# Optimization experiments

Measured on AMD Instinct MI355X. Metric: run time of the kernel, lower is better.

Reference implementation:

```python
import jax, jax.numpy as jnp
import numpy as np

N = 8192
D_IN = 128
D_OUT = 128


def setup_inputs() -> dict:
    key = jax.random.key(0)
    k1, k2, k3 = jax.random.split(key, 3)
    x = jax.random.normal(k1, (N, D_IN), dtype=jnp.float32)
    adj = jax.random.uniform(k2, (N, N), dtype=jnp.float32)  # dense adjacency / edge weights
    weight = jax.random.normal(k3, (D_IN, D_OUT), dtype=jnp.float32) * (1.0 / np.sqrt(D_IN))
    bias = jnp.zeros((D_OUT,), dtype=jnp.float32)
    return {"x": x, "adj": adj, "weight": weight, "bias": bias}


def gcn_norm(adj, add_self_loops=False):
    # symmetric normalization: D^{-1/2} A D^{-1/2}
    if add_self_loops:
        adj = adj + jnp.eye(adj.shape[0], dtype=adj.dtype)
    deg = adj.sum(axis=1)
    dinv = jnp.where(deg > 0, jax.lax.rsqrt(deg), 0.0)  # masked_fill(isinf, 0)
    return adj * dinv[:, None] * dinv[None, :]


def reference(x, adj, weight, bias):
    adj_n = gcn_norm(adj, add_self_loops=False)  # cached normalized adjacency
    h = x @ weight                               # [N, D_out] dense projection
    out = adj_n @ h + bias                       # neighborhood aggregation + bias
    return out
```

## Files before the change

### kernel.cpp

```cpp
#include <hip/hip_runtime.h>
#include <hip/hip_bf16.h>

#define NN 8192
#define DD 128

typedef __attribute__((ext_vector_type(4))) float f32x4;
typedef __attribute__((ext_vector_type(8))) short s16x8;
typedef __attribute__((ext_vector_type(4))) short s16x4;

__device__ inline short bfbits(float f) {
    unsigned u = __builtin_bit_cast(unsigned, f);
    u += 0x7fffu + ((u >> 16) & 1u);
    return (short)(u >> 16);
}

__device__ inline s16x4 cvt4(f32x4 a) {
    s16x4 r;
    r[0] = bfbits(a[0]); r[1] = bfbits(a[1]); r[2] = bfbits(a[2]); r[3] = bfbits(a[3]);
    return r;
}

__device__ inline s16x8 cvt8(f32x4 a, f32x4 b) {
    s16x8 r;
    r[0] = bfbits(a[0]); r[1] = bfbits(a[1]); r[2] = bfbits(a[2]); r[3] = bfbits(a[3]);
    r[4] = bfbits(b[0]); r[5] = bfbits(b[1]); r[6] = bfbits(b[2]); r[7] = bfbits(b[3]);
    return r;
}

__global__ __launch_bounds__(256) void deg_kernel(const float* __restrict__ adj,
                                                  float* __restrict__ dinv) {
    const int lane = threadIdx.x & 63;
    const int row  = (blockIdx.x << 2) + (threadIdx.x >> 6);
    const float* r = adj + (size_t)row * NN;

    f32x4 s = {0.f, 0.f, 0.f, 0.f};
    #pragma unroll 4
    for (int it = 0; it < 32; ++it) {
        f32x4 v = *(const f32x4*)(r + it * 256 + (lane << 2));
        s += v;
    }
    float sum = s[0] + s[1] + s[2] + s[3];
    #pragma unroll
    for (int off = 32; off; off >>= 1) sum += __shfl_xor(sum, off, 64);
    if (lane == 0) dinv[row] = (sum > 0.f) ? rsqrtf(sum) : 0.f;
}

#define WST 132
__global__ __launch_bounds__(256) void proj_kernel(const float* __restrict__ x,
                                                   const float* __restrict__ w,
                                                   const float* __restrict__ dinv,
                                                   unsigned short* __restrict__ h2f) {
    __shared__ short lds_w[128 * WST];
    const int tid  = threadIdx.x;
    const int lane = tid & 63;
    const int wave = tid >> 6;
    const int j0   = blockIdx.x << 4;
    const int n0   = wave << 5;
    const int r    = lane & 15;
    const int q    = lane >> 4;

    #pragma unroll
    for (int i = 0; i < 16; ++i) {
        int gi = i * 256 + tid;
        int k  = gi >> 5;
        int n4 = (gi & 31) << 2;
        f32x4 v = *(const f32x4*)(w + (size_t)k * DD + n4);
        *(s16x4*)&lds_w[k * WST + n4] = cvt4(v);
    }
    __syncthreads();

    const float* xp = x + (size_t)(j0 + r) * DD + (q << 3);

    f32x4 acc0 = {0.f, 0.f, 0.f, 0.f};
    f32x4 acc1 = {0.f, 0.f, 0.f, 0.f};

    #pragma unroll
    for (int k = 0; k < DD; k += 32) {
        f32x4 a0 = *(const f32x4*)(xp + k);
        f32x4 a1 = *(const f32x4*)(xp + k + 4);
        s16x8 af = cvt8(a0, a1);

        const int kb = k + (q << 3);
        s16x8 b0, b1;
        #pragma unroll
        for (int jj = 0; jj < 8; ++jj) {
            b0[jj] = lds_w[(kb + jj) * WST + n0 + r];
            b1[jj] = lds_w[(kb + jj) * WST + n0 + 16 + r];
        }
        acc0 = __builtin_amdgcn_mfma_f32_16x16x32_bf16(af, b0, acc0, 0, 0, 0);
        acc1 = __builtin_amdgcn_mfma_f32_16x16x32_bf16(af, b1, acc1, 0, 0, 0);
    }

    #pragma unroll
    for (int rr = 0; rr < 4; ++rr) {
        const int j = j0 + (q << 2) + rr;
        const float dv = dinv[j];
        const int kg = j >> 5, qp = (j >> 3) & 3, jj = j & 7;
        #pragma unroll
        for (int half = 0; half < 2; ++half) {
            const int n = n0 + half * 16 + r;
            const int f = n >> 4;
            const int lanep = qp * 16 + (n & 15);
            const float v = (half ? acc1[rr] : acc0[rr]) * dv;
            h2f[((((size_t)f << 8) + kg) << 6 | lanep) * 8 + jj] = (unsigned short)bfbits(v);
        }
    }
}

template <int KSPLIT>
__global__ __launch_bounds__(256, 4) void agg32_kernel(const float* __restrict__ adj,
                                                       const unsigned short* __restrict__ h2f,
                                                       float* __restrict__ dst) {
    constexpr int KS    = NN / KSPLIT;
    constexpr int TILES = KS / 128;
    __shared__ short lds_a[2][2][16 * 16 * 8];

    const int tid  = threadIdx.x;
    const int lane = tid & 63;
    const int wave = tid >> 6;
    const int r    = lane & 15;
    const int q    = lane >> 4;
    const int m0   = blockIdx.x << 5;
    const int k0   = blockIdx.y * KS;

    const int row0 = tid >> 5;
    const int off0 = (tid & 31) << 2;
    const int cd   = (tid & 31) >> 1;
    const int hh   = tid & 1;
    const int so0  = ((row0 << 4) + (cd ^ row0)) * 8 + hh * 4;
    const int so1  = (((8 + row0) << 4) + (cd ^ (8 + row0))) * 8 + hh * 4;

    const float* ap0 = adj + (size_t)(m0 + row0)      * NN + k0 + off0;
    const float* ap1 = adj + (size_t)(m0 + 8 + row0)  * NN + k0 + off0;
    const float* ap2 = adj + (size_t)(m0 + 16 + row0) * NN + k0 + off0;
    const float* ap3 = adj + (size_t)(m0 + 24 + row0) * NN + k0 + off0;

    const unsigned short* bb0 = h2f + (((size_t)(wave * 2)     * 256 + (k0 >> 5)) * 64 + lane) * 8;
    const unsigned short* bb1 = h2f + (((size_t)(wave * 2 + 1) * 256 + (k0 >> 5)) * 64 + lane) * 8;

    f32x4 acc00 = {0.f, 0.f, 0.f, 0.f};
    f32x4 acc01 = {0.f, 0.f, 0.f, 0.f};
    f32x4 acc10 = {0.f, 0.f, 0.f, 0.f};
    f32x4 acc11 = {0.f, 0.f, 0.f, 0.f};

    {
        f32x4 v0 = *(const f32x4*)(ap0);
        f32x4 v1 = *(const f32x4*)(ap1);
        f32x4 v2 = *(const f32x4*)(ap2);
        f32x4 v3 = *(const f32x4*)(ap3);
        *(s16x4*)&lds_a[0][0][so0] = cvt4(v0);
        *(s16x4*)&lds_a[0][0][so1] = cvt4(v1);
        *(s16x4*)&lds_a[0][1][so0] = cvt4(v2);
        *(s16x4*)&lds_a[0][1][so1] = cvt4(v3);
    }
    __syncthreads();

    for (int t = 0; t < TILES; ++t) {
        const short* lc0 = lds_a[t & 1][0];
        const short* lc1 = lds_a[t & 1][1];

        s16x8 br0[4], br1[4];
        #pragma unroll
        for (int s = 0; s < 4; ++s) {
            br0[s] = *(const s16x8*)(bb0 + (size_t)(t * 4 + s) * 512);
            br1[s] = *(const s16x8*)(bb1 + (size_t)(t * 4 + s) * 512);
        }
        f32x4 v0, v1, v2, v3;
        if (t + 1 < TILES) {
            v0 = *(const f32x4*)(ap0 + (t + 1) * 128);
            v1 = *(const f32x4*)(ap1 + (t + 1) * 128);
            v2 = *(const f32x4*)(ap2 + (t + 1) * 128);
            v3 = *(const f32x4*)(ap3 + (t + 1) * 128);
        }
        #pragma unroll
        for (int s = 0; s < 4; ++s) {
            const int slot = (r << 4) + (((s << 2) + q) ^ r);
            s16x8 afA = *(const s16x8*)(lc0 + slot * 8);
            s16x8 afB = *(const s16x8*)(lc1 + slot * 8);
            acc00 = __builtin_amdgcn_mfma_f32_16x16x32_bf16(afA, br0[s], acc00, 0, 0, 0);
            acc01 = __builtin_amdgcn_mfma_f32_16x16x32_bf16(afA, br1[s], acc01, 0, 0, 0);
            acc10 = __builtin_amdgcn_mfma_f32_16x16x32_bf16(afB, br0[s], acc10, 0, 0, 0);
            acc11 = __builtin_amdgcn_mfma_f32_16x16x32_bf16(afB, br1[s], acc11, 0, 0, 0);
        }
        if (t + 1 < TILES) {
            short* ln0 = (short*)lds_a[(t + 1) & 1][0];
            short* ln1 = (short*)lds_a[(t + 1) & 1][1];
            *(s16x4*)(ln0 + so0) = cvt4(v0);
            *(s16x4*)(ln0 + so1) = cvt4(v1);
            *(s16x4*)(ln1 + so0) = cvt4(v2);
            *(s16x4*)(ln1 + so1) = cvt4(v3);
        }
        __syncthreads();
    }

    float* p = dst + (size_t)blockIdx.y * NN * DD;
    #pragma unroll
    for (int rr = 0; rr < 4; ++rr) {
        const int mA = m0 + (q << 2) + rr;
        const int mB = mA + 16;
        const int n  = (wave << 5) + r;
        p[(size_t)mA * DD + n]      = acc00[rr];
        p[(size_t)mA * DD + n + 16] = acc01[rr];
        p[(size_t)mB * DD + n]      = acc10[rr];
        p[(size_t)mB * DD + n + 16] = acc11[rr];
    }
}

template <int KSPLIT>
__global__ __launch_bounds__(256, 4) void agg_kernel(const float* __restrict__ adj,
                                                     const unsigned short* __restrict__ h2f,
                                                     const float* __restrict__ dinv,
                                                     const float* __restrict__ bias,
                                                     float* __restrict__ dst) {
    constexpr int KS    = NN / KSPLIT;
    constexpr int TILES = KS / 128;
    __shared__ short lds_a[2][16 * 16 * 8];

    const int tid  = threadIdx.x;
    const int lane = tid & 63;
    const int wave = tid >> 6;
    const int r    = lane & 15;
    const int q    = lane >> 4;
    const int m0   = blockIdx.x << 4;
    const int k0   = blockIdx.y * KS;

    const int row0 = tid >> 5;
    const int off0 = (tid & 31) << 2;
    const int cd   = (tid & 31) >> 1;
    const int hh   = tid & 1;
    const int so0  = ((row0 << 4) + (cd ^ row0)) * 8 + hh * 4;
    const int so1  = (((8 + row0) << 4) + (cd ^ (8 + row0))) * 8 + hh * 4;

    const float* ap0 = adj + (size_t)(m0 + row0) * NN + k0 + off0;
    const float* ap1 = adj + (size_t)(m0 + 8 + row0) * NN + k0 + off0;

    const unsigned short* bb0 = h2f + (((size_t)(wave * 2)     * 256 + (k0 >> 5)) * 64 + lane) * 8;
    const unsigned short* bb1 = h2f + (((size_t)(wave * 2 + 1) * 256 + (k0 >> 5)) * 64 + lane) * 8;

    f32x4 acc0 = {0.f, 0.f, 0.f, 0.f};
    f32x4 acc1 = {0.f, 0.f, 0.f, 0.f};

    {
        f32x4 v0 = *(const f32x4*)(ap0);
        f32x4 v1 = *(const f32x4*)(ap1);
        *(s16x4*)&lds_a[0][so0] = cvt4(v0);
        *(s16x4*)&lds_a[0][so1] = cvt4(v1);
    }
    __syncthreads();

    for (int t = 0; t < TILES; ++t) {
        const short* lcur = lds_a[t & 1];
        short* lnxt = (short*)lds_a[(t + 1) & 1];

        s16x8 br0[4], br1[4];
        #pragma unroll
        for (int s = 0; s < 4; ++s) {
            br0[s] = *(const s16x8*)(bb0 + (size_t)(t * 4 + s) * 512);
            br1[s] = *(const s16x8*)(bb1 + (size_t)(t * 4 + s) * 512);
        }
        f32x4 v0, v1;
        if (t + 1 < TILES) {
            v0 = *(const f32x4*)(ap0 + (t + 1) * 128);
            v1 = *(const f32x4*)(ap1 + (t + 1) * 128);
        }
        #pragma unroll
        for (int s = 0; s < 4; ++s) {
            const int slot = (r << 4) + (((s << 2) + q) ^ r);
            s16x8 af = *(const s16x8*)(lcur + slot * 8);
            acc0 = __builtin_amdgcn_mfma_f32_16x16x32_bf16(af, br0[s], acc0, 0, 0, 0);
            acc1 = __builtin_amdgcn_mfma_f32_16x16x32_bf16(af, br1[s], acc1, 0, 0, 0);
        }
        if (t + 1 < TILES) {
            *(s16x4*)(lnxt + so0) = cvt4(v0);
            *(s16x4*)(lnxt + so1) = cvt4(v1);
        }
        __syncthreads();
    }

    #pragma unroll
    for (int rr = 0; rr < 4; ++rr) {
        const int m = m0 + (q << 2) + rr;
        const int n = (wave << 5) + r;
        if (KSPLIT == 1) {
            const float dv = dinv[m];
            dst[(size_t)m * DD + n]      = acc0[rr] * dv + bias[n];
            dst[(size_t)m * DD + n + 16] = acc1[rr] * dv + bias[n + 16];
        } else {
            float* p = dst + (size_t)blockIdx.y * NN * DD;
            p[(size_t)m * DD + n]      = acc0[rr];
            p[(size_t)m * DD + n + 16] = acc1[rr];
        }
    }
}

__global__ __launch_bounds__(256) void reduce4_kernel(const float* __restrict__ part,
                                                      const float* __restrict__ dinv,
                                                      const float* __restrict__ bias,
                                                      float* __restrict__ out) {
    const int idx = blockIdx.x * 256 + threadIdx.x;
    const f32x4 a = ((const f32x4*)part)[idx];
    const f32x4 b = ((const f32x4*)part)[idx + NN * DD / 4];
    const f32x4 c = ((const f32x4*)part)[idx + 2 * (NN * DD / 4)];
    const f32x4 d = ((const f32x4*)part)[idx + 3 * (NN * DD / 4)];
    const float dv = dinv[idx >> 5];
    const f32x4 bi = *(const f32x4*)(bias + ((idx & 31) << 2));
    f32x4 s = (a + b) + (c + d);
    f32x4 o;
    o[0] = s[0] * dv + bi[0]; o[1] = s[1] * dv + bi[1];
    o[2] = s[2] * dv + bi[2]; o[3] = s[3] * dv + bi[3];
    ((f32x4*)out)[idx] = o;
}

__global__ __launch_bounds__(256) void reduce_kernel(const float* __restrict__ part,
                                                     const float* __restrict__ dinv,
                                                     const float* __restrict__ bias,
                                                     float* __restrict__ out) {
    const int idx = blockIdx.x * 256 + threadIdx.x;
    const f32x4 a = ((const f32x4*)part)[idx];
    const f32x4 b = ((const f32x4*)part)[idx + NN * DD / 4];
    const float dv = dinv[idx >> 5];
    const f32x4 bi = *(const f32x4*)(bias + ((idx & 31) << 2));
    f32x4 s = a + b;
    f32x4 o;
    o[0] = s[0] * dv + bi[0]; o[1] = s[1] * dv + bi[1];
    o[2] = s[2] * dv + bi[2]; o[3] = s[3] * dv + bi[3];
    ((f32x4*)out)[idx] = o;
}

extern "C" void kernel_launch(void* const* d_in, const int* in_sizes, int n_in,
                              void* d_out, int out_size, void* d_ws, size_t ws_size,
                              hipStream_t stream) {
    const float* x    = (const float*)d_in[0];
    const float* adj  = (const float*)d_in[1];
    const float* w    = (const float*)d_in[2];
    const float* bias = (const float*)d_in[3];
    float* out = (float*)d_out;

    float* dinv = (float*)d_ws;
    unsigned short* h2f = (unsigned short*)((char*)d_ws + 32 * 1024);
    float* part = (float*)((char*)d_ws + 32 * 1024 + 2 * 1024 * 1024);
    const size_t base  = 32 * 1024 + 2 * 1024 * 1024;
    const size_t need4 = base + (size_t)4 * NN * DD * sizeof(float);
    const size_t need2 = base + (size_t)2 * NN * DD * sizeof(float);

    deg_kernel<<<NN / 4, 256, 0, stream>>>(adj, dinv);
    proj_kernel<<<NN / 16, 256, 0, stream>>>(x, w, dinv, h2f);

    if (ws_size >= need4) {
        agg32_kernel<4><<<dim3(NN / 32, 4), 256, 0, stream>>>(adj, h2f, part);
        reduce4_kernel<<<NN * DD / 4 / 256, 256, 0, stream>>>(part, dinv, bias, out);
    } else if (ws_size >= need2) {
        agg_kernel<2><<<dim3(NN / 16, 2), 256, 0, stream>>>(adj, h2f, dinv, bias, part);
        reduce_kernel<<<NN * DD / 4 / 256, 256, 0, stream>>>(part, dinv, bias, out);
    } else {
        agg_kernel<1><<<dim3(NN / 16, 1), 256, 0, stream>>>(adj, h2f, dinv, bias, out);
    }
}
```

Before: 425.6 us.

## Fuse degree and projection into one prep kernel, scale by dinv afterwards

The degree reduction and the x@W projection are merged into one launch whose blocks are split by index, so the projection no longer waits for the degree pass. The projection writes unscaled fp32 results to a new workspace buffer, and a small scale kernel then applies dinv and converts to bf16 in the blocked layout. This removes the serial dependency between the two prep kernels at the cost of an extra launch and an extra 4 MB fp32 write and read. The new path is used only when the workspace is large enough, otherwise the old paths are kept.

```diff
diff --git a/kernel.cpp b/kernel.cpp
--- a/kernel.cpp
+++ b/kernel.cpp
@@ -27,84 +27,103 @@
     return r;
 }
 
-__global__ __launch_bounds__(256) void deg_kernel(const float* __restrict__ adj,
-                                                  float* __restrict__ dinv) {
-    const int lane = threadIdx.x & 63;
-    const int row  = (blockIdx.x << 2) + (threadIdx.x >> 6);
-    const float* r = adj + (size_t)row * NN;
-
-    f32x4 s = {0.f, 0.f, 0.f, 0.f};
-    #pragma unroll 4
-    for (int it = 0; it < 32; ++it) {
-        f32x4 v = *(const f32x4*)(r + it * 256 + (lane << 2));
-        s += v;
-    }
-    float sum = s[0] + s[1] + s[2] + s[3];
-    #pragma unroll
-    for (int off = 32; off; off >>= 1) sum += __shfl_xor(sum, off, 64);
-    if (lane == 0) dinv[row] = (sum > 0.f) ? rsqrtf(sum) : 0.f;
-}
-
 #define WST 132
-__global__ __launch_bounds__(256) void proj_kernel(const float* __restrict__ x,
+
+__global__ __launch_bounds__(256) void prep_kernel(const float* __restrict__ adj,
+                                                   const float* __restrict__ x,
                                                    const float* __restrict__ w,
-                                                   const float* __restrict__ dinv,
-                                                   unsigned short* __restrict__ h2f) {
+                                                   float* __restrict__ dinv,
+                                                   float* __restrict__ hU) {
     __shared__ short lds_w[128 * WST];
-    const int tid  = threadIdx.x;
-    const int lane = tid & 63;
-    const int wave = tid >> 6;
-    const int j0   = blockIdx.x << 4;
-    const int n0   = wave << 5;
-    const int r    = lane & 15;
-    const int q    = lane >> 4;
-
-    #pragma unroll
-    for (int i = 0; i < 16; ++i) {
-        int gi = i * 256 + tid;
-        int k  = gi >> 5;
-        int n4 = (gi & 31) << 2;
-        f32x4 v = *(const f32x4*)(w + (size_t)k * DD + n4);
-        *(s16x4*)&lds_w[k * WST + n4] = cvt4(v);
-    }
-    __syncthreads();
-
-    const float* xp = x + (size_t)(j0 + r) * DD + (q << 3);
-
-    f32x4 acc0 = {0.f, 0.f, 0.f, 0.f};
-    f32x4 acc1 = {0.f, 0.f, 0.f, 0.f};
-
-    #pragma unroll
-    for (int k = 0; k < DD; k += 32) {
-        f32x4 a0 = *(const f32x4*)(xp + k);
-        f32x4 a1 = *(const f32x4*)(xp + k + 4);
-        s16x8 af = cvt8(a0, a1);
-
-        const int kb = k + (q << 3);
-        s16x8 b0, b1;
-        #pragma unroll
-        for (int jj = 0; jj < 8; ++jj) {
-            b0[jj] = lds_w[(kb + jj) * WST + n0 + r];
-            b1[jj] = lds_w[(kb + jj) * WST + n0 + 16 + r];
-        }
-        acc0 = __builtin_amdgcn_mfma_f32_16x16x32_bf16(af, b0, acc0, 0, 0, 0);
-        acc1 = __builtin_amdgcn_mfma_f32_16x16x32_bf16(af, b1, acc1, 0, 0, 0);
-    }
-
-    #pragma unroll
-    for (int rr = 0; rr < 4; ++rr) {
-        const int j = j0 + (q << 2) + rr;
-        const float dv = dinv[j];
-        const int kg = j >> 5, qp = (j >> 3) & 3, jj = j & 7;
-        #pragma unroll
-        for (int half = 0; half < 2; ++half) {
-            const int n = n0 + half * 16 + r;
-            const int f = n >> 4;
-            const int lanep = qp * 16 + (n & 15);
-            const float v = (half ? acc1[rr] : acc0[rr]) * dv;
-            h2f[((((size_t)f << 8) + kg) << 6 | lanep) * 8 + jj] = (unsigned short)bfbits(v);
-        }
-    }
+    const int tid = threadIdx.x;
+
+    if (blockIdx.x < 2048) {
+        const int lane = tid & 63;
+        const int row  = (blockIdx.x << 2) + (tid >> 6);
+        const float* r = adj + (size_t)row * NN;
+
+        f32x4 s = {0.f, 0.f, 0.f, 0.f};
+        #pragma unroll 4
+        for (int it = 0; it < 32; ++it) {
+            f32x4 v = *(const f32x4*)(r + it * 256 + (lane << 2));
+            s += v;
+        }
+        float sum = s[0] + s[1] + s[2] + s[3];
+        #pragma unroll
+        for (int off = 32; off; off >>= 1) sum += __shfl_xor(sum, off, 64);
+        if (lane == 0) dinv[row] = (sum > 0.f) ? rsqrtf(sum) : 0.f;
+    } else {
+        const int pb   = blockIdx.x - 2048;
+        const int lane = tid & 63;
+        const int wave = tid >> 6;
+        const int j0   = pb << 4;
+        const int n0   = wave << 5;
+        const int r    = lane & 15;
+        const int q    = lane >> 4;
+
+        #pragma unroll
+        for (int i = 0; i < 16; ++i) {
+            int gi = i * 256 + tid;
+            int k  = gi >> 5;
+            int n4 = (gi & 31) << 2;
+            f32x4 v = *(const f32x4*)(w + (size_t)k * DD + n4);
+            *(s16x4*)&lds_w[k * WST + n4] = cvt4(v);
+        }
+        __syncthreads();
+
+        const float* xp = x + (size_t)(j0 + r) * DD + (q << 3);
+        f32x4 acc0 = {0.f, 0.f, 0.f, 0.f};
+        f32x4 acc1 = {0.f, 0.f, 0.f, 0.f};
+
+        #pragma unroll
+        for (int k = 0; k < DD; k += 32) {
+            f32x4 a0 = *(const f32x4*)(xp + k);
+            f32x4 a1 = *(const f32x4*)(xp + k + 4);
+            s16x8 af = cvt8(a0, a1);
+            const int kb = k + (q << 3);
+            s16x8 b0, b1;
+            #pragma unroll
+            for (int jj = 0; jj < 8; ++jj) {
+                b0[jj] = lds_w[(kb + jj) * WST + n0 + r];
+                b1[jj] = lds_w[(kb + jj) * WST + n0 + 16 + r];
+            }
+            acc0 = __builtin_amdgcn_mfma_f32_16x16x32_bf16(af, b0, acc0, 0, 0, 0);
+            acc1 = __builtin_amdgcn_mfma_f32_16x16x32_bf16(af, b1, acc1, 0, 0, 0);
+        }
+
+        #pragma unroll
+        for (int rr = 0; rr < 4; ++rr) {
+            const int j  = j0 + (q << 2) + rr;
+            const int kg = j >> 5, qp = (j >> 3) & 3, jj = j & 7;
+            #pragma unroll
+            for (int half = 0; half < 2; ++half) {
+                const int n = n0 + half * 16 + r;
+                const int f = n >> 4;
+                const int lanep = qp * 16 + (n & 15);
+                hU[(((size_t)((f << 8) | kg) << 6) | lanep) * 8 + jj] =
+                    (half ? acc1[rr] : acc0[rr]);
+            }
+        }
+    }
+}
+
+__global__ __launch_bounds__(256) void scale_kernel(const float* __restrict__ hU,
+                                                    const float* __restrict__ dinv,
+                                                    unsigned short* __restrict__ h2f) {
+    const int s  = blockIdx.x * 256 + threadIdx.x;
+    const int kg = (s >> 6) & 255;
+    const int qp = (s >> 4) & 3;
+    const int j0 = (kg << 5) + (qp << 3);
+    f32x4 a  = *(const f32x4*)(hU + (size_t)s * 8);
+    f32x4 b  = *(const f32x4*)(hU + (size_t)s * 8 + 4);
+    f32x4 d0 = *(const f32x4*)(dinv + j0);
+    f32x4 d1 = *(const f32x4*)(dinv + j0 + 4);
+    s16x8 o;
+    o[0] = bfbits(a[0] * d0[0]); o[1] = bfbits(a[1] * d0[1]);
+    o[2] = bfbits(a[2] * d0[2]); o[3] = bfbits(a[3] * d0[3]);
+    o[4] = bfbits(b[0] * d1[0]); o[5] = bfbits(b[1] * d1[1]);
+    o[6] = bfbits(b[2] * d1[2]); o[7] = bfbits(b[3] * d1[3]);
+    *(s16x8*)(h2f + (size_t)s * 8) = o;
 }
 
 template <int KSPLIT>
@@ -203,93 +222,6 @@
         p[(size_t)mA * DD + n + 16] = acc01[rr];
         p[(size_t)mB * DD + n]      = acc10[rr];
         p[(size_t)mB * DD + n + 16] = acc11[rr];
-    }
-}
-
-template <int KSPLIT>
-__global__ __launch_bounds__(256, 4) void agg_kernel(const float* __restrict__ adj,
-                                                     const unsigned short* __restrict__ h2f,
-                                                     const float* __restrict__ dinv,
-                                                     const float* __restrict__ bias,
-                                                     float* __restrict__ dst) {
-    constexpr int KS    = NN / KSPLIT;
-    constexpr int TILES = KS / 128;
-    __shared__ short lds_a[2][16 * 16 * 8];
-
-    const int tid  = threadIdx.x;
-    const int lane = tid & 63;
-    const int wave = tid >> 6;
-    const int r    = lane & 15;
-    const int q    = lane >> 4;
-    const int m0   = blockIdx.x << 4;
-    const int k0   = blockIdx.y * KS;
-
-    const int row0 = tid >> 5;
-    const int off0 = (tid & 31) << 2;
-    const int cd   = (tid & 31) >> 1;
-    const int hh   = tid & 1;
-    const int so0  = ((row0 << 4) + (cd ^ row0)) * 8 + hh * 4;
-    const int so1  = (((8 + row0) << 4) + (cd ^ (8 + row0))) * 8 + hh * 4;
-
-    const float* ap0 = adj + (size_t)(m0 + row0) * NN + k0 + off0;
-    const float* ap1 = adj + (size_t)(m0 + 8 + row0) * NN + k0 + off0;
-
-    const unsigned short* bb0 = h2f + (((size_t)(wave * 2)     * 256 + (k0 >> 5)) * 64 + lane) * 8;
-    const unsigned short* bb1 = h2f + (((size_t)(wave * 2 + 1) * 256 + (k0 >> 5)) * 64 + lane) * 8;
-
-    f32x4 acc0 = {0.f, 0.f, 0.f, 0.f};
-    f32x4 acc1 = {0.f, 0.f, 0.f, 0.f};
-
-    {
-        f32x4 v0 = *(const f32x4*)(ap0);
-        f32x4 v1 = *(const f32x4*)(ap1);
-        *(s16x4*)&lds_a[0][so0] = cvt4(v0);
-        *(s16x4*)&lds_a[0][so1] = cvt4(v1);
-    }
-    __syncthreads();
-
-    for (int t = 0; t < TILES; ++t) {
-        const short* lcur = lds_a[t & 1];
-        short* lnxt = (short*)lds_a[(t + 1) & 1];
-
-        s16x8 br0[4], br1[4];
-        #pragma unroll
-        for (int s = 0; s < 4; ++s) {
-            br0[s] = *(const s16x8*)(bb0 + (size_t)(t * 4 + s) * 512);
-            br1[s] = *(const s16x8*)(bb1 + (size_t)(t * 4 + s) * 512);
-        }
-        f32x4 v0, v1;
-        if (t + 1 < TILES) {
-            v0 = *(const f32x4*)(ap0 + (t + 1) * 128);
-            v1 = *(const f32x4*)(ap1 + (t + 1) * 128);
-        }
-        #pragma unroll
-        for (int s = 0; s < 4; ++s) {
-            const int slot = (r << 4) + (((s << 2) + q) ^ r);
-            s16x8 af = *(const s16x8*)(lcur + slot * 8);
-            acc0 = __builtin_amdgcn_mfma_f32_16x16x32_bf16(af, br0[s], acc0, 0, 0, 0);
-            acc1 = __builtin_amdgcn_mfma_f32_16x16x32_bf16(af, br1[s], acc1, 0, 0, 0);
-        }
-        if (t + 1 < TILES) {
-            *(s16x4*)(lnxt + so0) = cvt4(v0);
-            *(s16x4*)(lnxt + so1) = cvt4(v1);
-        }
-        __syncthreads();
-    }
-
-    #pragma unroll
-    for (int rr = 0; rr < 4; ++rr) {
-        const int m = m0 + (q << 2) + rr;
-        const int n = (wave << 5) + r;
-        if (KSPLIT == 1) {
-            const float dv = dinv[m];
-            dst[(size_t)m * DD + n]      = acc0[rr] * dv + bias[n];
-            dst[(size_t)m * DD + n + 16] = acc1[rr] * dv + bias[n + 16];
-        } else {
-            float* p = dst + (size_t)blockIdx.y * NN * DD;
-            p[(size_t)m * DD + n]      = acc0[rr];
-            p[(size_t)m * DD + n + 16] = acc1[rr];
-        }
     }
 }
 
@@ -311,6 +243,156 @@
     ((f32x4*)out)[idx] = o;
 }
 
+__global__ __launch_bounds__(256) void deg_kernel(const float* __restrict__ adj,
+                                                  float* __restrict__ dinv) {
+    const int lane = threadIdx.x & 63;
+    const int row  = (blockIdx.x << 2) + (threadIdx.x >> 6);
+    const float* r = adj + (size_t)row * NN;
+    f32x4 s = {0.f, 0.f, 0.f, 0.f};
+    #pragma unroll 4
+    for (int it = 0; it < 32; ++it) {
+        f32x4 v = *(const f32x4*)(r + it * 256 + (lane << 2));
+        s += v;
+    }
+    float sum = s[0] + s[1] + s[2] + s[3];
+    #pragma unroll
+    for (int off = 32; off; off >>= 1) sum += __shfl_xor(sum, off, 64);
+    if (lane == 0) dinv[row] = (sum > 0.f) ? rsqrtf(sum) : 0.f;
+}
+
+__global__ __launch_bounds__(256) void proj_kernel(const float* __restrict__ x,
+                                                   const float* __restrict__ w,
+                                                   const float* __restrict__ dinv,
+                                                   unsigned short* __restrict__ h2f) {
+    __shared__ short lds_w[128 * WST];
+    const int tid  = threadIdx.x;
+    const int lane = tid & 63;
+    const int wave = tid >> 6;
+    const int j0   = blockIdx.x << 4;
+    const int n0   = wave << 5;
+    const int r    = lane & 15;
+    const int q    = lane >> 4;
+    #pragma unroll
+    for (int i = 0; i < 16; ++i) {
+        int gi = i * 256 + tid;
+        int k  = gi >> 5;
+        int n4 = (gi & 31) << 2;
+        f32x4 v = *(const f32x4*)(w + (size_t)k * DD + n4);
+        *(s16x4*)&lds_w[k * WST + n4] = cvt4(v);
+    }
+    __syncthreads();
+    const float* xp = x + (size_t)(j0 + r) * DD + (q << 3);
+    f32x4 acc0 = {0.f, 0.f, 0.f, 0.f};
+    f32x4 acc1 = {0.f, 0.f, 0.f, 0.f};
+    #pragma unroll
+    for (int k = 0; k < DD; k += 32) {
+        f32x4 a0 = *(const f32x4*)(xp + k);
+        f32x4 a1 = *(const f32x4*)(xp + k + 4);
+        s16x8 af = cvt8(a0, a1);
+        const int kb = k + (q << 3);
+        s16x8 b0, b1;
+        #pragma unroll
+        for (int jj = 0; jj < 8; ++jj) {
+            b0[jj] = lds_w[(kb + jj) * WST + n0 + r];
+            b1[jj] = lds_w[(kb + jj) * WST + n0 + 16 + r];
+        }
+        acc0 = __builtin_amdgcn_mfma_f32_16x16x32_bf16(af, b0, acc0, 0, 0, 0);
+        acc1 = __builtin_amdgcn_mfma_f32_16x16x32_bf16(af, b1, acc1, 0, 0, 0);
+    }
+    #pragma unroll
+    for (int rr = 0; rr < 4; ++rr) {
+        const int j = j0 + (q << 2) + rr;
+        const float dv = dinv[j];
+        const int kg = j >> 5, qp = (j >> 3) & 3, jj = j & 7;
+        #pragma unroll
+        for (int half = 0; half < 2; ++half) {
+            const int n = n0 + half * 16 + r;
+            const int f = n >> 4;
+            const int lanep = qp * 16 + (n & 15);
+            const float v = (half ? acc1[rr] : acc0[rr]) * dv;
+            h2f[((((size_t)f << 8) + kg) << 6 | lanep) * 8 + jj] = (unsigned short)bfbits(v);
+        }
+    }
+}
+
+template <int KSPLIT>
+__global__ __launch_bounds__(256, 4) void agg_kernel(const float* __restrict__ adj,
+                                                     const unsigned short* __restrict__ h2f,
+                                                     const float* __restrict__ dinv,
+                                                     const float* __restrict__ bias,
+                                                     float* __restrict__ dst) {
+    constexpr int KS    = NN / KSPLIT;
+    constexpr int TILES = KS / 128;
+    __shared__ short lds_a[2][16 * 16 * 8];
+    const int tid  = threadIdx.x;
+    const int lane = tid & 63;
+    const int wave = tid >> 6;
+    const int r    = lane & 15;
+    const int q    = lane >> 4;
+    const int m0   = blockIdx.x << 4;
+    const int k0   = blockIdx.y * KS;
+    const int row0 = tid >> 5;
+    const int off0 = (tid & 31) << 2;
+    const int cd   = (tid & 31) >> 1;
+    const int hh   = tid & 1;
+    const int so0  = ((row0 << 4) + (cd ^ row0)) * 8 + hh * 4;
+    const int so1  = (((8 + row0) << 4) + (cd ^ (8 + row0))) * 8 + hh * 4;
+    const float* ap0 = adj + (size_t)(m0 + row0) * NN + k0 + off0;
+    const float* ap1 = adj + (size_t)(m0 + 8 + row0) * NN + k0 + off0;
+    const unsigned short* bb0 = h2f + (((size_t)(wave * 2)     * 256 + (k0 >> 5)) * 64 + lane) * 8;
+    const unsigned short* bb1 = h2f + (((size_t)(wave * 2 + 1) * 256 + (k0 >> 5)) * 64 + lane) * 8;
+    f32x4 acc0 = {0.f, 0.f, 0.f, 0.f};
+    f32x4 acc1 = {0.f, 0.f, 0.f, 0.f};
+    {
+        f32x4 v0 = *(const f32x4*)(ap0);
+        f32x4 v1 = *(const f32x4*)(ap1);
+        *(s16x4*)&lds_a[0][so0] = cvt4(v0);
+        *(s16x4*)&lds_a[0][so1] = cvt4(v1);
+    }
+    __syncthreads();
+    for (int t = 0; t < TILES; ++t) {
+        const short* lcur = lds_a[t & 1];
+        short* lnxt = (short*)lds_a[(t + 1) & 1];
+        s16x8 br0[4], br1[4];
+        #pragma unroll
+        for (int s = 0; s < 4; ++s) {
+            br0[s] = *(const s16x8*)(bb0 + (size_t)(t * 4 + s) * 512);
+            br1[s] = *(const s16x8*)(bb1 + (size_t)(t * 4 + s) * 512);
+        }
+        f32x4 v0, v1;
+        if (t + 1 < TILES) {
+            v0 = *(const f32x4*)(ap0 + (t + 1) * 128);
+            v1 = *(const f32x4*)(ap1 + (t + 1) * 128);
+        }
+        #pragma unroll
+        for (int s = 0; s < 4; ++s) {
+            const int slot = (r << 4) + (((s << 2) + q) ^ r);
+            s16x8 af = *(const s16x8*)(lcur + slot * 8);
+            acc0 = __builtin_amdgcn_mfma_f32_16x16x32_bf16(af, br0[s], acc0, 0, 0, 0);
+            acc1 = __builtin_amdgcn_mfma_f32_16x16x32_bf16(af, br1[s], acc1, 0, 0, 0);
+        }
+        if (t + 1 < TILES) {
+            *(s16x4*)(lnxt + so0) = cvt4(v0);
+            *(s16x4*)(lnxt + so1) = cvt4(v1);
+        }
+        __syncthreads();
+    }
+    #pragma unroll
+    for (int rr = 0; rr < 4; ++rr) {
+        const int m = m0 + (q << 2) + rr;
+        const int n = (wave << 5) + r;
+        if (KSPLIT == 1) {
+            const float dv = dinv[m];
+            dst[(size_t)m * DD + n]      = acc0[rr] * dv + bias[n];
+            dst[(size_t)m * DD + n + 16] = acc1[rr] * dv + bias[n + 16];
+        } else {
+            float* p = dst + (size_t)blockIdx.y * NN * DD;
+            p[(size_t)m * DD + n]      = acc0[rr];
+            p[(size_t)m * DD + n + 16] = acc1[rr];
+        }
+    }
+}
+
 __global__ __launch_bounds__(256) void reduce_kernel(const float* __restrict__ part,
                                                      const float* __restrict__ dinv,
                                                      const float* __restrict__ bias,
@@ -336,23 +418,36 @@
     const float* bias = (const float*)d_in[3];
     float* out = (float*)d_out;
 
-    float* dinv = (float*)d_ws;
+    float* dinv         = (float*)d_ws;
     unsigned short* h2f = (unsigned short*)((char*)d_ws + 32 * 1024);
-    float* part = (float*)((char*)d_ws + 32 * 1024 + 2 * 1024 * 1024);
-    const size_t base  = 32 * 1024 + 2 * 1024 * 1024;
-    const size_t need4 = base + (size_t)4 * NN * DD * sizeof(float);
-    const size_t need2 = base + (size_t)2 * NN * DD * sizeof(float);
-
-    deg_kernel<<<NN / 4, 256, 0, stream>>>(adj, dinv);
-    proj_kernel<<<NN / 16, 256, 0, stream>>>(x, w, dinv, h2f);
-
-    if (ws_size >= need4) {
+    float* hU           = (float*)((char*)d_ws + 32 * 1024 + 2 * 1024 * 1024);
+    float* part         = (float*)((char*)d_ws + 32 * 1024 + 6 * 1024 * 1024);
+    const size_t base_f = 32 * 1024 + 6 * 1024 * 1024;
+    const size_t need_fused = base_f + (size_t)4 * NN * DD * sizeof(float);
+    const size_t base_s = 32 * 1024 + 2 * 1024 * 1024;
+    const size_t need4  = base_s + (size_t)4 * NN * DD * sizeof(float);
+    const size_t need2  = base_s + (size_t)2 * NN * DD * sizeof(float);
+
+    if (ws_size >= need_fused) {
+        prep_kernel<<<2560, 256, 0, stream>>>(adj, x, w, dinv, hU);
+        scale_kernel<<<512, 256, 0, stream>>>(hU, dinv, h2f);
         agg32_kernel<4><<<dim3(NN / 32, 4), 256, 0, stream>>>(adj, h2f, part);
         reduce4_kernel<<<NN * DD / 4 / 256, 256, 0, stream>>>(part, dinv, bias, out);
+    } else if (ws_size >= need4) {
+        float* part_s = (float*)((char*)d_ws + base_s);
+        deg_kernel<<<NN / 4, 256, 0, stream>>>(adj, dinv);
+        proj_kernel<<<NN / 16, 256, 0, stream>>>(x, w, dinv, h2f);
+        agg32_kernel<4><<<dim3(NN / 32, 4), 256, 0, stream>>>(adj, h2f, part_s);
+        reduce4_kernel<<<NN * DD / 4 / 256, 256, 0, stream>>>(part_s, dinv, bias, out);
     } else if (ws_size >= need2) {
-        agg_kernel<2><<<dim3(NN / 16, 2), 256, 0, stream>>>(adj, h2f, dinv, bias, part);
-        reduce_kernel<<<NN * DD / 4 / 256, 256, 0, stream>>>(part, dinv, bias, out);
+        float* part_s = (float*)((char*)d_ws + base_s);
+        deg_kernel<<<NN / 4, 256, 0, stream>>>(adj, dinv);
+        proj_kernel<<<NN / 16, 256, 0, stream>>>(x, w, dinv, h2f);
+        agg_kernel<2><<<dim3(NN / 16, 2), 256, 0, stream>>>(adj, h2f, dinv, bias, part_s);
+        reduce_kernel<<<NN * DD / 4 / 256, 256, 0, stream>>>(part_s, dinv, bias, out);
     } else {
+        deg_kernel<<<NN / 4, 256, 0, stream>>>(adj, dinv);
+        proj_kernel<<<NN / 16, 256, 0, stream>>>(x, w, dinv, h2f);
         agg_kernel<1><<<dim3(NN / 16, 1), 256, 0, stream>>>(adj, h2f, dinv, bias, out);
     }
 }
```

Measured after the change: 425.9 us. No clear change (+0.1%).
